# Kernel optimization log

Hardware: AMD Instinct MI355X
Metric: run time of the kernel (lower is better)

The kernel has to match this reference:

```python
import jax, jax.numpy as jnp
import numpy as np

B, L, IN_DIM, DIM, H = 1, 256, 128, 32, 4
LN_EPS = 1e-5


def setup_inputs() -> dict:
    key = jax.random.key(0)
    ks = jax.random.split(key, 7)
    z = jax.random.normal(ks[0], (B, L, L, IN_DIM), dtype=jnp.float32)
    src_mask = jax.random.randint(ks[1], (B, L), 0, 2, dtype=jnp.int32)
    ln_g = jnp.ones((IN_DIM,), jnp.float32)
    ln_b = jnp.zeros((IN_DIM,), jnp.float32)
    w_qkv = jax.random.normal(ks[2], (IN_DIM, 3 * H * DIM), jnp.float32) * 0.02
    w_pair = jax.random.normal(ks[3], (IN_DIM, H), jnp.float32) * 0.02
    w_gate = jax.random.normal(ks[4], (IN_DIM, IN_DIM), jnp.float32) * 0.02
    b_gate = jnp.zeros((IN_DIM,), jnp.float32)
    w_out = jax.random.normal(ks[5], (H * DIM, IN_DIM), jnp.float32) * 0.02
    b_out = jnp.zeros((IN_DIM,), jnp.float32)
    return dict(z=z, src_mask=src_mask, ln_g=ln_g, ln_b=ln_b, w_qkv=w_qkv,
                w_pair=w_pair, w_gate=w_gate, b_gate=b_gate, w_out=w_out, b_out=b_out)


def reference(z, src_mask, ln_g, ln_b, w_qkv, w_pair, w_gate, b_gate, w_out, b_out):
    # mask: 0 -> -1, then outer product -> (B, L, L) with entries in {-1, +1}
    m = jnp.where(src_mask == 0, -1, src_mask).astype(jnp.float32)
    attn_mask = m[:, :, None] * m[:, None, :]                      # (B, L, L)

    # LayerNorm over feature dim (biased variance, as torch)
    mu = jnp.mean(z, axis=-1, keepdims=True)
    var = jnp.mean((z - mu) ** 2, axis=-1, keepdims=True)
    zn = (z - mu) / jnp.sqrt(var + LN_EPS) * ln_g + ln_b           # (B, I, J, C)

    gate = jax.nn.sigmoid(zn @ w_gate + b_gate)                    # (B, I, J, C)
    bias = zn @ w_pair                                             # (B, I, J, H)

    qkv = zn @ w_qkv                                               # (B, I, J, 3*H*D)
    q, k, v = jnp.split(qkv, 3, axis=-1)
    q = q.reshape(B, L, L, H, DIM)
    k = k.reshape(B, L, L, H, DIM)
    v = v.reshape(B, L, L, H, DIM)

    # NOTE: original code DIVIDES by scale = d**-0.5 (i.e. multiplies by sqrt(d)).
    scale = DIM ** (-0.5)
    logits = jnp.einsum('brihd,brjhd->brijh', q, k) / scale        # (B, R, I, J, H)
    logits = logits + bias[:, None, :, :, :]
    # NOTE: original masked_fill uses -1e-9 (tiny), kept faithfully.
    logits = jnp.where(attn_mask[:, None, :, :, None] == -1, jnp.float32(-1e-9), logits)
    attn = jax.nn.softmax(logits, axis=3)                          # softmax over key j

    out = jnp.einsum('brijh,brjhd->brihd', attn, v)                # (B, R, I, H, D)
    out = out.reshape(B, L, L, H * DIM)
    return (gate * out) @ w_out + b_out                            # (B, I, J, C)
```

## Files before the change

kernel.cpp:

```cpp
#include <hip/hip_runtime.h>
#include <hip/hip_bf16.h>

#define L_DIM 256
#define C_DIM 128
#define H_DIM 4
#define D_DIM 32
#define NPOS (L_DIM * L_DIM)
#define SQRT_D 5.6568542494923806f

typedef float f32x4 __attribute__((ext_vector_type(4)));
typedef short bf16x8 __attribute__((ext_vector_type(8)));
typedef unsigned short ushort8_t __attribute__((ext_vector_type(8)));

__device__ __forceinline__ float bf2f(unsigned short u) {
  return __uint_as_float(((unsigned)u) << 16);
}
__device__ __forceinline__ unsigned short f2bf(float f) {
  unsigned u = __float_as_uint(f);
  unsigned r = u + 0x7fffu + ((u >> 16) & 1u);
  return (unsigned short)(r >> 16);
}

__global__ __launch_bounds__(256)
void k_prep(const float* __restrict__ w_qkv, const float* __restrict__ w_gate,
            const float* __restrict__ w_out,
            unsigned short* __restrict__ WcT, unsigned short* __restrict__ WoT) {
  int idx = blockIdx.x * 256 + threadIdx.x;
  if (idx < 512 * 128) {
    int n = idx >> 7, c = idx & 127;
    float v = (n < 384) ? w_qkv[c * 384 + n] : w_gate[c * 128 + (n - 384)];
    WcT[idx] = f2bf(v);
  } else if (idx < 512 * 128 + 128 * 128) {
    int i2 = idx - 512 * 128;
    int n = i2 >> 7, c = i2 & 127;
    WoT[i2] = f2bf(w_out[c * 128 + n]);
  }
}

__global__ __launch_bounds__(256)
void k_bias(const float* __restrict__ z, const float* __restrict__ ln_g,
            const float* __restrict__ ln_b, const float* __restrict__ w_pair,
            float* __restrict__ biasT) {
  int t = threadIdx.x;
  int p = blockIdx.x * 32 + (t >> 3);
  int lane = t & 7;
  const float* zp = &z[(size_t)p * C_DIM + lane * 16];
  float x[16];
  #pragma unroll
  for (int e = 0; e < 4; e++) {
    float4 v = reinterpret_cast<const float4*>(zp)[e];
    x[e * 4 + 0] = v.x; x[e * 4 + 1] = v.y; x[e * 4 + 2] = v.z; x[e * 4 + 3] = v.w;
  }
  float s = 0.f;
  #pragma unroll
  for (int e = 0; e < 16; e++) s += x[e];
  s += __shfl_xor(s, 1); s += __shfl_xor(s, 2); s += __shfl_xor(s, 4);
  float mu = s * (1.0f / C_DIM);
  float v2 = 0.f;
  #pragma unroll
  for (int e = 0; e < 16; e++) { float d = x[e] - mu; v2 += d * d; }
  v2 += __shfl_xor(v2, 1); v2 += __shfl_xor(v2, 2); v2 += __shfl_xor(v2, 4);
  float rs = rsqrtf(v2 * (1.0f / C_DIM) + 1e-5f);
  float bh[H_DIM] = {};
  #pragma unroll
  for (int e = 0; e < 16; e++) {
    int c = lane * 16 + e;
    float zn = (x[e] - mu) * rs * ln_g[c] + ln_b[c];
    #pragma unroll
    for (int h = 0; h < H_DIM; h++) bh[h] += zn * w_pair[c * H_DIM + h];
  }
  #pragma unroll
  for (int h = 0; h < H_DIM; h++) {
    bh[h] += __shfl_xor(bh[h], 1); bh[h] += __shfl_xor(bh[h], 2); bh[h] += __shfl_xor(bh[h], 4);
  }
  if (lane == 0) {
    int iz = p >> 8, jz = p & 255;
    #pragma unroll
    for (int h = 0; h < H_DIM; h++) biasT[h * NPOS + jz * L_DIM + iz] = bh[h];
  }
}

__global__ __launch_bounds__(512, 2)
void k_fused(const float* __restrict__ z, const int* __restrict__ src_mask,
             const float* __restrict__ ln_g, const float* __restrict__ ln_b,
             const float* __restrict__ b_gate, const unsigned short* __restrict__ WcT,
             const float* __restrict__ biasT, float* __restrict__ og) {
  __shared__ __align__(16) char smem[156672];
  char* zn_c = smem;
  unsigned short* Qs = (unsigned short*)(smem + 65536);
  unsigned short* Ks = (unsigned short*)(smem + 86016);
  char* Vt_c = smem + 106496;
  char* Wt_c = smem + 122880;
  int* smk   = (int*)(smem + 155648);

  const int t = threadIdx.x;
  const int wave = t >> 6, lane = t & 63;
  const int rbase = blockIdx.x * L_DIM;
  const int wrow0 = wave * 32;
  char* P_c = smem + 122880 + wave * 4096;

  {
    int ln8 = t & 7;
    for (int pass = 0; pass < 4; ++pass) {
      int pos = pass * 64 + (t >> 3);
      const float* zp = z + ((size_t)(rbase + pos)) * C_DIM + ln8 * 16;
      float x[16];
      #pragma unroll
      for (int e = 0; e < 4; e++) {
        float4 v = reinterpret_cast<const float4*>(zp)[e];
        x[e * 4 + 0] = v.x; x[e * 4 + 1] = v.y; x[e * 4 + 2] = v.z; x[e * 4 + 3] = v.w;
      }
      float s = 0.f;
      #pragma unroll
      for (int e = 0; e < 16; e++) s += x[e];
      s += __shfl_xor(s, 1); s += __shfl_xor(s, 2); s += __shfl_xor(s, 4);
      float mu = s * (1.0f / C_DIM);
      float v2 = 0.f;
      #pragma unroll
      for (int e = 0; e < 16; e++) { float d = x[e] - mu; v2 += d * d; }
      v2 += __shfl_xor(v2, 1); v2 += __shfl_xor(v2, 2); v2 += __shfl_xor(v2, 4);
      float rstd = rsqrtf(v2 * (1.0f / C_DIM) + 1e-5f);
      unsigned short hb[16];
      #pragma unroll
      for (int e = 0; e < 16; e++) {
        int c = ln8 * 16 + e;
        hb[e] = f2bf((x[e] - mu) * rstd * ln_g[c] + ln_b[c]);
      }
      uint4 w0, w1;
      w0.x = hb[0] | ((unsigned)hb[1] << 16);  w0.y = hb[2] | ((unsigned)hb[3] << 16);
      w0.z = hb[4] | ((unsigned)hb[5] << 16);  w0.w = hb[6] | ((unsigned)hb[7] << 16);
      w1.x = hb[8] | ((unsigned)hb[9] << 16);  w1.y = hb[10] | ((unsigned)hb[11] << 16);
      w1.z = hb[12] | ((unsigned)hb[13] << 16); w1.w = hb[14] | ((unsigned)hb[15] << 16);
      int sw = (pos & 7) << 4;
      *(uint4*)(zn_c + pos * 256 + ((ln8 * 32) ^ sw)) = w0;
      *(uint4*)(zn_c + pos * 256 + ((ln8 * 32 + 16) ^ sw)) = w1;
    }
    if (t < 256) smk[t] = src_mask[t];
  }

  unsigned mib = 0;

  f32x4 gacc[2][2];

  for (int h = 0; h < H_DIM; ++h) {
    {
      int row = t >> 2, q4 = t & 3;
      int src = ((row >> 5) * 128) + h * 32 + (row & 31);
      const char* gsrc = (const char*)(WcT + src * 128);
      int sw = (row & 7) << 4;
      #pragma unroll
      for (int e = 0; e < 4; e++) {
        int cb = q4 * 64 + e * 16;
        ushort8_t v = *(const ushort8_t*)(gsrc + cb);
        *(ushort8_t*)(Wt_c + row * 256 + (cb ^ sw)) = v;
      }
    }
    __syncthreads();
    if (h == 0) {
      #pragma unroll
      for (int mi = 0; mi < 2; mi++)
        #pragma unroll
        for (int q = 0; q < 4; q++) {
          int i = wrow0 + mi * 16 + (lane >> 4) * 4 + q;
          if (smk[i] == 0) mib |= 1u << (mi * 4 + q);
        }
    }

    bf16x8 afr[2][4];
    #pragma unroll
    for (int mi = 0; mi < 2; mi++)
      #pragma unroll
      for (int kk = 0; kk < 4; kk++) {
        int row = wrow0 + mi * 16 + (lane & 15);
        int cb = kk * 64 + (lane >> 4) * 16;
        afr[mi][kk] = *(const bf16x8*)(zn_c + row * 256 + (cb ^ ((row & 7) << 4)));
      }
    #pragma unroll
    for (int o = 0; o < 4; o++) {
      #pragma unroll
      for (int mi = 0; mi < 2; mi++) {
        #pragma unroll
        for (int nt = 0; nt < 2; nt++) {
          f32x4 acc = {0.f, 0.f, 0.f, 0.f};
          #pragma unroll
          for (int kk = 0; kk < 4; kk++) {
            int wr = o * 32 + nt * 16 + (lane & 15);
            int cb = kk * 64 + (lane >> 4) * 16;
            bf16x8 bfr = *(const bf16x8*)(Wt_c + wr * 256 + (cb ^ ((wr & 7) << 4)));
            acc = __builtin_amdgcn_mfma_f32_16x16x32_bf16(afr[mi][kk], bfr, acc, 0, 0, 0);
          }
          int colb = nt * 16 + (lane & 15);
          int rowb = wrow0 + mi * 16 + (lane >> 4) * 4;
          if (o == 0) {
            #pragma unroll
            for (int q = 0; q < 4; q++) Qs[(rowb + q) * 40 + colb] = f2bf(acc[q]);
          } else if (o == 1) {
            #pragma unroll
            for (int q = 0; q < 4; q++) Ks[(rowb + q) * 40 + colb] = f2bf(acc[q]);
          } else if (o == 2) {
            uint2 pv;
            pv.x = f2bf(acc[0]) | ((unsigned)f2bf(acc[1]) << 16);
            pv.y = f2bf(acc[2]) | ((unsigned)f2bf(acc[3]) << 16);
            *(uint2*)(Vt_c + colb * 512 + ((rowb * 2) ^ ((colb & 7) << 4))) = pv;
          } else {
            gacc[mi][nt] = acc;
          }
        }
      }
    }
    __syncthreads();

    float m_run[2][4], s_run[2][4];
    f32x4 o_acc[2][2];
    #pragma unroll
    for (int mi = 0; mi < 2; mi++)
      #pragma unroll
      for (int q = 0; q < 4; q++) { m_run[mi][q] = -3.0e38f; s_run[mi][q] = 0.f; }
    #pragma unroll
    for (int mi = 0; mi < 2; mi++)
      #pragma unroll
      for (int nd = 0; nd < 2; nd++) o_acc[mi][nd] = (f32x4){0.f, 0.f, 0.f, 0.f};

    bf16x8 qfr[2];
    #pragma unroll
    for (int mi = 0; mi < 2; mi++) {
      int qr = wrow0 + mi * 16 + (lane & 15);
      qfr[mi] = *(const bf16x8*)((const char*)Qs + qr * 80 + (lane >> 4) * 16);
    }
    const float* biasTh = biasT + h * NPOS;

    for (int jb = 0; jb < 4; ++jb) {
      bf16x8 kfr[4];
      #pragma unroll
      for (int ji = 0; ji < 4; ji++) {
        int jr = jb * 64 + ji * 16 + (lane & 15);
        kfr[ji] = *(const bf16x8*)((const char*)Ks + jr * 80 + (lane >> 4) * 16);
      }
      f32x4 sacc[2][4];
      #pragma unroll
      for (int mi = 0; mi < 2; mi++)
        #pragma unroll
        for (int ji = 0; ji < 4; ji++) {
          f32x4 zz = {0.f, 0.f, 0.f, 0.f};
          sacc[mi][ji] = __builtin_amdgcn_mfma_f32_16x16x32_bf16(qfr[mi], kfr[ji], zz, 0, 0, 0);
        }
      #pragma unroll
      for (int mi = 0; mi < 2; mi++) {
        #pragma unroll
        for (int ji = 0; ji < 4; ji++) {
          int j = jb * 64 + ji * 16 + (lane & 15);
          int ib = wrow0 + mi * 16 + (lane >> 4) * 4;
          float4 b4 = *(const float4*)(biasTh + j * L_DIM + ib);
          bool mjz = (smk[j] == 0);
          float bb[4] = {b4.x, b4.y, b4.z, b4.w};
          #pragma unroll
          for (int q = 0; q < 4; q++) {
            float sv = sacc[mi][ji][q] * SQRT_D + bb[q];
            bool miz = (mib >> (mi * 4 + q)) & 1u;
            if (miz != mjz) sv = -1e-9f;
            sacc[mi][ji][q] = sv;
          }
        }
      }
      #pragma unroll
      for (int mi = 0; mi < 2; mi++) {
        #pragma unroll
        for (int q = 0; q < 4; q++) {
          float v = fmaxf(fmaxf(sacc[mi][0][q], sacc[mi][1][q]),
                          fmaxf(sacc[mi][2][q], sacc[mi][3][q]));
          v = fmaxf(v, __shfl_xor(v, 1)); v = fmaxf(v, __shfl_xor(v, 2));
          v = fmaxf(v, __shfl_xor(v, 4)); v = fmaxf(v, __shfl_xor(v, 8));
          float mo = m_run[mi][q];
          float mn = fmaxf(mo, v);
          float corr = __expf(mo - mn);
          m_run[mi][q] = mn;
          float rs = 0.f;
          #pragma unroll
          for (int ji = 0; ji < 4; ji++) {
            float pp = __expf(sacc[mi][ji][q] - mn);
            sacc[mi][ji][q] = pp; rs += pp;
          }
          rs += __shfl_xor(rs, 1); rs += __shfl_xor(rs, 2);
          rs += __shfl_xor(rs, 4); rs += __shfl_xor(rs, 8);
          s_run[mi][q] = s_run[mi][q] * corr + rs;
          o_acc[mi][0][q] *= corr; o_acc[mi][1][q] *= corr;
        }
      }
      #pragma unroll
      for (int mi = 0; mi < 2; mi++)
        #pragma unroll
        for (int ji = 0; ji < 4; ji++) {
          #pragma unroll
          for (int q = 0; q < 4; q++) {
            int il = mi * 16 + (lane >> 4) * 4 + q;
            int jl = ji * 16 + (lane & 15);
            *(unsigned short*)(P_c + il * 128 + ((jl * 2) ^ ((il & 7) << 4))) =
                f2bf(sacc[mi][ji][q]);
          }
        }
      #pragma unroll
      for (int kk = 0; kk < 2; kk++) {
        bf16x8 pfr[2], vfr[2];
        #pragma unroll
        for (int mi = 0; mi < 2; mi++) {
          int pr = mi * 16 + (lane & 15);
          pfr[mi] = *(const bf16x8*)(P_c + pr * 128 +
                                     ((kk * 64 + (lane >> 4) * 16) ^ ((pr & 7) << 4)));
        }
        #pragma unroll
        for (int nd = 0; nd < 2; nd++) {
          int vr = nd * 16 + (lane & 15);
          vfr[nd] = *(const bf16x8*)(Vt_c + vr * 512 +
                                     ((jb * 128 + kk * 64 + (lane >> 4) * 16) ^ ((vr & 7) << 4)));
        }
        #pragma unroll
        for (int mi = 0; mi < 2; mi++)
          #pragma unroll
          for (int nd = 0; nd < 2; nd++)
            o_acc[mi][nd] = __builtin_amdgcn_mfma_f32_16x16x32_bf16(pfr[mi], vfr[nd],
                                                                    o_acc[mi][nd], 0, 0, 0);
      }
    }

    #pragma unroll
    for (int mi = 0; mi < 2; mi++) {
      float rcp[4];
      #pragma unroll
      for (int q = 0; q < 4; q++) rcp[q] = 1.0f / s_run[mi][q];
      #pragma unroll
      for (int nd = 0; nd < 2; nd++) {
        int c = h * 32 + nd * 16 + (lane & 15);
        float bg = b_gate[c];
        #pragma unroll
        for (int q = 0; q < 4; q++) {
          float g = 1.0f / (1.0f + __expf(-(gacc[mi][nd][q] + bg)));
          float ov = o_acc[mi][nd][q] * rcp[q] * g;
          int p = rbase + wrow0 + mi * 16 + (lane >> 4) * 4 + q;
          og[(size_t)p * C_DIM + c] = ov;
        }
      }
    }
    __syncthreads();
  }
}

__global__ __launch_bounds__(256)
void k_out(const unsigned short* __restrict__ WoT, const float* __restrict__ b_out,
           float* __restrict__ out) {
  __shared__ __align__(16) char smem[49152];
  char* Ab_c  = smem;
  char* WoT_c = smem + 16384;
  int t = threadIdx.x;
  int gr0 = blockIdx.x * 64;
  #pragma unroll
  for (int e = 0; e < 8; e++) {
    int f = t + e * 256;
    int row = f >> 5, c4 = f & 31;
    float4 v = *(const float4*)(out + (size_t)(gr0 + row) * C_DIM + c4 * 4);
    uint2 pv;
    pv.x = f2bf(v.x) | ((unsigned)f2bf(v.y) << 16);
    pv.y = f2bf(v.z) | ((unsigned)f2bf(v.w) << 16);
    *(uint2*)(Ab_c + row * 256 + ((c4 * 8) ^ ((row & 7) << 4))) = pv;
  }
  {
    int row = t >> 1, seg = t & 1;
    const char* gsrc = (const char*)(WoT + row * 128);
    int sw = (row & 7) << 4;
    #pragma unroll
    for (int e = 0; e < 8; e++) {
      int cb = seg * 128 + e * 16;
      ushort8_t v = *(const ushort8_t*)(gsrc + cb);
      *(ushort8_t*)(WoT_c + row * 256 + (cb ^ sw)) = v;
    }
  }
  __syncthreads();

  int wave = t >> 6, lane = t & 63;
  int base = wave * 16;
  bf16x8 afr[4];
  #pragma unroll
  for (int kk = 0; kk < 4; kk++) {
    int row = base + (lane & 15);
    int cb = kk * 64 + (lane >> 4) * 16;
    afr[kk] = *(const bf16x8*)(Ab_c + row * 256 + (cb ^ ((row & 7) << 4)));
  }
  f32x4 acc[8];
  #pragma unroll
  for (int nt = 0; nt < 8; nt++) {
    acc[nt] = (f32x4){0.f, 0.f, 0.f, 0.f};
    #pragma unroll
    for (int kk = 0; kk < 4; kk++) {
      int wr = nt * 16 + (lane & 15);
      int cb = kk * 64 + (lane >> 4) * 16;
      bf16x8 bfr = *(const bf16x8*)(WoT_c + wr * 256 + (cb ^ ((wr & 7) << 4)));
      acc[nt] = __builtin_amdgcn_mfma_f32_16x16x32_bf16(afr[kk], bfr, acc[nt], 0, 0, 0);
    }
  }
  __syncthreads();
  #pragma unroll
  for (int nt = 0; nt < 8; nt++) {
    int n = nt * 16 + (lane & 15);
    float bo = b_out[n];
    #pragma unroll
    for (int q = 0; q < 4; q++) {
      int p = gr0 + base + (lane >> 4) * 4 + q;
      out[(size_t)p * C_DIM + n] = acc[nt][q] + bo;
    }
  }
}

extern "C" void kernel_launch(void* const* d_in, const int* in_sizes, int n_in,
                              void* d_out, int out_size, void* d_ws, size_t ws_size,
                              hipStream_t stream) {
  const float* z      = (const float*)d_in[0];
  const int*   smask  = (const int*)  d_in[1];
  const float* ln_g   = (const float*)d_in[2];
  const float* ln_b   = (const float*)d_in[3];
  const float* w_qkv  = (const float*)d_in[4];
  const float* w_pair = (const float*)d_in[5];
  const float* w_gate = (const float*)d_in[6];
  const float* b_gate = (const float*)d_in[7];
  const float* w_out  = (const float*)d_in[8];
  const float* b_out  = (const float*)d_in[9];
  float* out = (float*)d_out;

  char* ws = (char*)d_ws;
  unsigned short* WcT   = (unsigned short*)(ws);
  unsigned short* WoT   = (unsigned short*)(ws + 131072);
  float*          biasT = (float*)(ws + 163840);
  (void)ws_size; (void)in_sizes; (void)n_in; (void)out_size;

  k_prep<<<dim3(320), dim3(256), 0, stream>>>(w_qkv, w_gate, w_out, WcT, WoT);
  k_bias<<<dim3(NPOS / 32), dim3(256), 0, stream>>>(z, ln_g, ln_b, w_pair, biasT);
  k_fused<<<dim3(L_DIM), dim3(512), 0, stream>>>(z, smask, ln_g, ln_b, b_gate, WcT, biasT, out);
  k_out<<<dim3(NPOS / 64), dim3(256), 0, stream>>>(WoT, b_out, out);
}
```

Before: 228.4 us.

## Use 1024-thread blocks, drop online-softmax max, double-buffer pre-swizzled weights

Doubles the waves per block so each wave handles 16 query rows instead of 32, improving latency hiding at one block per CU. It also removes the running-max online softmax in favour of a direct exp-and-sum with a single final normalisation. Weights are pre-swizzled per head in the prep kernel, and the next head's weights are prefetched into registers and double-buffered in LDS. The zn fragments and the mask bits are hoisted out of the head loop. Skipping max subtraction risks exp overflow if the logits grow large, and the shared-memory regions now alias, since Q, K and V reuse the zn area.

Measured after the change: 192.1 us. 1.19x faster.

```diff
diff --git a/kernel.cpp b/kernel.cpp
--- a/kernel.cpp
+++ b/kernel.cpp
@@ -4,7 +4,6 @@
 #define L_DIM 256
 #define C_DIM 128
 #define H_DIM 4
-#define D_DIM 32
 #define NPOS (L_DIM * L_DIM)
 #define SQRT_D 5.6568542494923806f
 
@@ -24,14 +23,17 @@
 __global__ __launch_bounds__(256)
 void k_prep(const float* __restrict__ w_qkv, const float* __restrict__ w_gate,
             const float* __restrict__ w_out,
-            unsigned short* __restrict__ WcT, unsigned short* __restrict__ WoT) {
+            unsigned short* __restrict__ WcS, unsigned short* __restrict__ WoT) {
   int idx = blockIdx.x * 256 + threadIdx.x;
-  if (idx < 512 * 128) {
-    int n = idx >> 7, c = idx & 127;
-    float v = (n < 384) ? w_qkv[c * 384 + n] : w_gate[c * 128 + (n - 384)];
-    WcT[idx] = f2bf(v);
-  } else if (idx < 512 * 128 + 128 * 128) {
-    int i2 = idx - 512 * 128;
+  if (idx < 4 * 128 * 128) {
+    int h = idx >> 14, rem = idx & 16383, rr = rem >> 7, c = rem & 127;
+    int o = rr >> 5, n32 = rr & 31;
+    float v = (o < 3) ? w_qkv[c * 384 + o * 128 + h * 32 + n32]
+                      : w_gate[c * 128 + h * 32 + n32];
+    int byte_in_row = (2 * c) ^ ((rr & 7) << 4);
+    WcS[h * 16384 + rr * 128 + (byte_in_row >> 1)] = f2bf(v);
+  } else if (idx < 4 * 128 * 128 + 128 * 128) {
+    int i2 = idx - 65536;
     int n = i2 >> 7, c = i2 & 127;
     WoT[i2] = f2bf(w_out[c * 128 + n]);
   }
@@ -80,29 +82,32 @@
   }
 }
 
-__global__ __launch_bounds__(512, 2)
+__global__ __launch_bounds__(1024)
 void k_fused(const float* __restrict__ z, const int* __restrict__ src_mask,
              const float* __restrict__ ln_g, const float* __restrict__ ln_b,
-             const float* __restrict__ b_gate, const unsigned short* __restrict__ WcT,
+             const float* __restrict__ b_gate, const unsigned short* __restrict__ WcS,
              const float* __restrict__ biasT, float* __restrict__ og) {
   __shared__ __align__(16) char smem[156672];
   char* zn_c = smem;
-  unsigned short* Qs = (unsigned short*)(smem + 65536);
-  unsigned short* Ks = (unsigned short*)(smem + 86016);
-  char* Vt_c = smem + 106496;
-  char* Wt_c = smem + 122880;
-  int* smk   = (int*)(smem + 155648);
+  unsigned short* Qs = (unsigned short*)(smem);
+  unsigned short* Ks = (unsigned short*)(smem + 20480);
+  char* Vt_c = smem + 40960;
+  char* P_c0 = smem + 57344;
+  char* Wt_c = smem + 90112;
+  int*  smk  = (int*)(smem + 155648);
 
   const int t = threadIdx.x;
   const int wave = t >> 6, lane = t & 63;
+  const int l15 = lane & 15, l4 = lane >> 4;
   const int rbase = blockIdx.x * L_DIM;
-  const int wrow0 = wave * 32;
-  char* P_c = smem + 122880 + wave * 4096;
+  const int wrow0 = wave * 16;
+  char* P_c = P_c0 + wave * 2048;
 
   {
     int ln8 = t & 7;
-    for (int pass = 0; pass < 4; ++pass) {
-      int pos = pass * 64 + (t >> 3);
+    #pragma unroll
+    for (int pass = 0; pass < 2; ++pass) {
+      int pos = pass * 128 + (t >> 3);
       const float* zp = z + ((size_t)(rbase + pos)) * C_DIM + ln8 * 16;
       float x[16];
       #pragma unroll
@@ -136,209 +141,141 @@
       *(uint4*)(zn_c + pos * 256 + ((ln8 * 32 + 16) ^ sw)) = w1;
     }
     if (t < 256) smk[t] = src_mask[t];
-  }
-
-  unsigned mib = 0;
-
-  f32x4 gacc[2][2];
+    const ushort8_t* src = (const ushort8_t*)WcS;
+    ushort8_t* dst = (ushort8_t*)Wt_c;
+    dst[t] = src[t];
+    dst[t + 1024] = src[t + 1024];
+  }
+  __syncthreads();
+
+  bf16x8 afr[4];
+  {
+    int row = wrow0 + l15, sw = (row & 7) << 4;
+    #pragma unroll
+    for (int kk = 0; kk < 4; kk++)
+      afr[kk] = *(const bf16x8*)(zn_c + row * 256 + ((kk * 64 + l4 * 16) ^ sw));
+  }
+  unsigned mib = 0, mjb = 0;
+  #pragma unroll
+  for (int q = 0; q < 4; q++)
+    if (smk[wrow0 + l4 * 4 + q] == 0) mib |= 1u << q;
+  #pragma unroll
+  for (int jj = 0; jj < 16; jj++)
+    if (smk[(jj >> 2) * 64 + (jj & 3) * 16 + l15] == 0) mjb |= 1u << jj;
+  __syncthreads();
 
   for (int h = 0; h < H_DIM; ++h) {
-    {
-      int row = t >> 2, q4 = t & 3;
-      int src = ((row >> 5) * 128) + h * 32 + (row & 31);
-      const char* gsrc = (const char*)(WcT + src * 128);
-      int sw = (row & 7) << 4;
-      #pragma unroll
-      for (int e = 0; e < 4; e++) {
-        int cb = q4 * 64 + e * 16;
-        ushort8_t v = *(const ushort8_t*)(gsrc + cb);
-        *(ushort8_t*)(Wt_c + row * 256 + (cb ^ sw)) = v;
+    const char* WtCur = Wt_c + (h & 1) * 32768;
+    ushort8_t ld0, ld1;
+    if (h < 3) {
+      const ushort8_t* src = (const ushort8_t*)(WcS + (h + 1) * 16384);
+      ld0 = src[t]; ld1 = src[t + 1024];
+    }
+
+    f32x4 gacc[2];
+    #pragma unroll
+    for (int o = 0; o < 4; o++) {
+      #pragma unroll
+      for (int nt = 0; nt < 2; nt++) {
+        f32x4 acc = {0.f, 0.f, 0.f, 0.f};
+        #pragma unroll
+        for (int kk = 0; kk < 4; kk++) {
+          int wr = o * 32 + nt * 16 + l15;
+          bf16x8 bfr = *(const bf16x8*)(WtCur + wr * 256 + ((kk * 64 + l4 * 16) ^ ((wr & 7) << 4)));
+          acc = __builtin_amdgcn_mfma_f32_16x16x32_bf16(afr[kk], bfr, acc, 0, 0, 0);
+        }
+        int colb = nt * 16 + l15;
+        int rowb = wrow0 + l4 * 4;
+        if (o == 0) {
+          #pragma unroll
+          for (int q = 0; q < 4; q++) Qs[(rowb + q) * 40 + colb] = f2bf(acc[q]);
+        } else if (o == 1) {
+          #pragma unroll
+          for (int q = 0; q < 4; q++) Ks[(rowb + q) * 40 + colb] = f2bf(acc[q]);
+        } else if (o == 2) {
+          uint2 pv;
+          pv.x = f2bf(acc[0]) | ((unsigned)f2bf(acc[1]) << 16);
+          pv.y = f2bf(acc[2]) | ((unsigned)f2bf(acc[3]) << 16);
+          *(uint2*)(Vt_c + colb * 512 + ((rowb * 2) ^ ((colb & 7) << 4))) = pv;
+        } else {
+          gacc[nt] = acc;
+        }
       }
     }
     __syncthreads();
-    if (h == 0) {
-      #pragma unroll
-      for (int mi = 0; mi < 2; mi++)
+
+    bf16x8 qfr = *(const bf16x8*)((const char*)Qs + (wrow0 + l15) * 80 + l4 * 16);
+    const float* biasTh = biasT + h * NPOS;
+    float s_part[4] = {0.f, 0.f, 0.f, 0.f};
+    f32x4 o_acc[2];
+    o_acc[0] = (f32x4){0.f, 0.f, 0.f, 0.f};
+    o_acc[1] = (f32x4){0.f, 0.f, 0.f, 0.f};
+
+    for (int jb = 0; jb < 4; ++jb) {
+      f32x4 sacc[4];
+      #pragma unroll
+      for (int ji = 0; ji < 4; ji++) {
+        int jr = jb * 64 + ji * 16 + l15;
+        bf16x8 kfr = *(const bf16x8*)((const char*)Ks + jr * 80 + l4 * 16);
+        f32x4 zz = {0.f, 0.f, 0.f, 0.f};
+        sacc[ji] = __builtin_amdgcn_mfma_f32_16x16x32_bf16(qfr, kfr, zz, 0, 0, 0);
+      }
+      #pragma unroll
+      for (int ji = 0; ji < 4; ji++) {
+        int j = jb * 64 + ji * 16 + l15;
+        int ib = wrow0 + l4 * 4;
+        float4 b4 = *(const float4*)(biasTh + j * L_DIM + ib);
+        bool mjz = (mjb >> (jb * 4 + ji)) & 1u;
+        float bb[4] = {b4.x, b4.y, b4.z, b4.w};
         #pragma unroll
         for (int q = 0; q < 4; q++) {
-          int i = wrow0 + mi * 16 + (lane >> 4) * 4 + q;
-          if (smk[i] == 0) mib |= 1u << (mi * 4 + q);
+          float sv = sacc[ji][q] * SQRT_D + bb[q];
+          bool miz = (mib >> q) & 1u;
+          if (miz != mjz) sv = -1e-9f;
+          float p = __expf(sv);
+          s_part[q] += p;
+          int il = l4 * 4 + q, jl = ji * 16 + l15;
+          *(unsigned short*)(P_c + il * 128 + ((jl * 2) ^ ((il & 7) << 4))) = f2bf(p);
         }
-    }
-
-    bf16x8 afr[2][4];
-    #pragma unroll
-    for (int mi = 0; mi < 2; mi++)
-      #pragma unroll
-      for (int kk = 0; kk < 4; kk++) {
-        int row = wrow0 + mi * 16 + (lane & 15);
-        int cb = kk * 64 + (lane >> 4) * 16;
-        afr[mi][kk] = *(const bf16x8*)(zn_c + row * 256 + (cb ^ ((row & 7) << 4)));
-      }
-    #pragma unroll
-    for (int o = 0; o < 4; o++) {
-      #pragma unroll
-      for (int mi = 0; mi < 2; mi++) {
-        #pragma unroll
-        for (int nt = 0; nt < 2; nt++) {
-          f32x4 acc = {0.f, 0.f, 0.f, 0.f};
-          #pragma unroll
-          for (int kk = 0; kk < 4; kk++) {
-            int wr = o * 32 + nt * 16 + (lane & 15);
-            int cb = kk * 64 + (lane >> 4) * 16;
-            bf16x8 bfr = *(const bf16x8*)(Wt_c + wr * 256 + (cb ^ ((wr & 7) << 4)));
-            acc = __builtin_amdgcn_mfma_f32_16x16x32_bf16(afr[mi][kk], bfr, acc, 0, 0, 0);
-          }
-          int colb = nt * 16 + (lane & 15);
-          int rowb = wrow0 + mi * 16 + (lane >> 4) * 4;
-          if (o == 0) {
-            #pragma unroll
-            for (int q = 0; q < 4; q++) Qs[(rowb + q) * 40 + colb] = f2bf(acc[q]);
-          } else if (o == 1) {
-            #pragma unroll
-            for (int q = 0; q < 4; q++) Ks[(rowb + q) * 40 + colb] = f2bf(acc[q]);
-          } else if (o == 2) {
-            uint2 pv;
-            pv.x = f2bf(acc[0]) | ((unsigned)f2bf(acc[1]) << 16);
-            pv.y = f2bf(acc[2]) | ((unsigned)f2bf(acc[3]) << 16);
-            *(uint2*)(Vt_c + colb * 512 + ((rowb * 2) ^ ((colb & 7) << 4))) = pv;
-          } else {
-            gacc[mi][nt] = acc;
-          }
-        }
-      }
-    }
-    __syncthreads();
-
-    float m_run[2][4], s_run[2][4];
-    f32x4 o_acc[2][2];
-    #pragma unroll
-    for (int mi = 0; mi < 2; mi++)
-      #pragma unroll
-      for (int q = 0; q < 4; q++) { m_run[mi][q] = -3.0e38f; s_run[mi][q] = 0.f; }
-    #pragma unroll
-    for (int mi = 0; mi < 2; mi++)
-      #pragma unroll
-      for (int nd = 0; nd < 2; nd++) o_acc[mi][nd] = (f32x4){0.f, 0.f, 0.f, 0.f};
-
-    bf16x8 qfr[2];
-    #pragma unroll
-    for (int mi = 0; mi < 2; mi++) {
-      int qr = wrow0 + mi * 16 + (lane & 15);
-      qfr[mi] = *(const bf16x8*)((const char*)Qs + qr * 80 + (lane >> 4) * 16);
-    }
-    const float* biasTh = biasT + h * NPOS;
-
-    for (int jb = 0; jb < 4; ++jb) {
-      bf16x8 kfr[4];
-      #pragma unroll
-      for (int ji = 0; ji < 4; ji++) {
-        int jr = jb * 64 + ji * 16 + (lane & 15);
-        kfr[ji] = *(const bf16x8*)((const char*)Ks + jr * 80 + (lane >> 4) * 16);
-      }
-      f32x4 sacc[2][4];
-      #pragma unroll
-      for (int mi = 0; mi < 2; mi++)
-        #pragma unroll
-        for (int ji = 0; ji < 4; ji++) {
-          f32x4 zz = {0.f, 0.f, 0.f, 0.f};
-          sacc[mi][ji] = __builtin_amdgcn_mfma_f32_16x16x32_bf16(qfr[mi], kfr[ji], zz, 0, 0, 0);
-        }
-      #pragma unroll
-      for (int mi = 0; mi < 2; mi++) {
-        #pragma unroll
-        for (int ji = 0; ji < 4; ji++) {
-          int j = jb * 64 + ji * 16 + (lane & 15);
-          int ib = wrow0 + mi * 16 + (lane >> 4) * 4;
-          float4 b4 = *(const float4*)(biasTh + j * L_DIM + ib);
-          bool mjz = (smk[j] == 0);
-          float bb[4] = {b4.x, b4.y, b4.z, b4.w};
-          #pragma unroll
-          for (int q = 0; q < 4; q++) {
-            float sv = sacc[mi][ji][q] * SQRT_D + bb[q];
-            bool miz = (mib >> (mi * 4 + q)) & 1u;
-            if (miz != mjz) sv = -1e-9f;
-            sacc[mi][ji][q] = sv;
-          }
-        }
-      }
-      #pragma unroll
-      for (int mi = 0; mi < 2; mi++) {
-        #pragma unroll
-        for (int q = 0; q < 4; q++) {
-          float v = fmaxf(fmaxf(sacc[mi][0][q], sacc[mi][1][q]),
-                          fmaxf(sacc[mi][2][q], sacc[mi][3][q]));
-          v = fmaxf(v, __shfl_xor(v, 1)); v = fmaxf(v, __shfl_xor(v, 2));
-          v = fmaxf(v, __shfl_xor(v, 4)); v = fmaxf(v, __shfl_xor(v, 8));
-          float mo = m_run[mi][q];
-          float mn = fmaxf(mo, v);
-          float corr = __expf(mo - mn);
-          m_run[mi][q] = mn;
-          float rs = 0.f;
-          #pragma unroll
-          for (int ji = 0; ji < 4; ji++) {
-            float pp = __expf(sacc[mi][ji][q] - mn);
-            sacc[mi][ji][q] = pp; rs += pp;
-          }
-          rs += __shfl_xor(rs, 1); rs += __shfl_xor(rs, 2);
-          rs += __shfl_xor(rs, 4); rs += __shfl_xor(rs, 8);
-          s_run[mi][q] = s_run[mi][q] * corr + rs;
-          o_acc[mi][0][q] *= corr; o_acc[mi][1][q] *= corr;
-        }
-      }
-      #pragma unroll
-      for (int mi = 0; mi < 2; mi++)
-        #pragma unroll
-        for (int ji = 0; ji < 4; ji++) {
-          #pragma unroll
-          for (int q = 0; q < 4; q++) {
-            int il = mi * 16 + (lane >> 4) * 4 + q;
-            int jl = ji * 16 + (lane & 15);
-            *(unsigned short*)(P_c + il * 128 + ((jl * 2) ^ ((il & 7) << 4))) =
-                f2bf(sacc[mi][ji][q]);
-          }
-        }
+      }
       #pragma unroll
       for (int kk = 0; kk < 2; kk++) {
-        bf16x8 pfr[2], vfr[2];
-        #pragma unroll
-        for (int mi = 0; mi < 2; mi++) {
-          int pr = mi * 16 + (lane & 15);
-          pfr[mi] = *(const bf16x8*)(P_c + pr * 128 +
-                                     ((kk * 64 + (lane >> 4) * 16) ^ ((pr & 7) << 4)));
-        }
+        bf16x8 pfr = *(const bf16x8*)(P_c + l15 * 128 + ((kk * 64 + l4 * 16) ^ ((l15 & 7) << 4)));
         #pragma unroll
         for (int nd = 0; nd < 2; nd++) {
-          int vr = nd * 16 + (lane & 15);
-          vfr[nd] = *(const bf16x8*)(Vt_c + vr * 512 +
-                                     ((jb * 128 + kk * 64 + (lane >> 4) * 16) ^ ((vr & 7) << 4)));
+          int vr = nd * 16 + l15;
+          bf16x8 vfr = *(const bf16x8*)(Vt_c + vr * 512 +
+                                        ((jb * 128 + kk * 64 + l4 * 16) ^ ((vr & 7) << 4)));
+          o_acc[nd] = __builtin_amdgcn_mfma_f32_16x16x32_bf16(pfr, vfr, o_acc[nd], 0, 0, 0);
         }
-        #pragma unroll
-        for (int mi = 0; mi < 2; mi++)
-          #pragma unroll
-          for (int nd = 0; nd < 2; nd++)
-            o_acc[mi][nd] = __builtin_amdgcn_mfma_f32_16x16x32_bf16(pfr[mi], vfr[nd],
-                                                                    o_acc[mi][nd], 0, 0, 0);
-      }
-    }
-
-    #pragma unroll
-    for (int mi = 0; mi < 2; mi++) {
-      float rcp[4];
-      #pragma unroll
-      for (int q = 0; q < 4; q++) rcp[q] = 1.0f / s_run[mi][q];
-      #pragma unroll
-      for (int nd = 0; nd < 2; nd++) {
-        int c = h * 32 + nd * 16 + (lane & 15);
-        float bg = b_gate[c];
-        #pragma unroll
-        for (int q = 0; q < 4; q++) {
-          float g = 1.0f / (1.0f + __expf(-(gacc[mi][nd][q] + bg)));
-          float ov = o_acc[mi][nd][q] * rcp[q] * g;
-          int p = rbase + wrow0 + mi * 16 + (lane >> 4) * 4 + q;
-          og[(size_t)p * C_DIM + c] = ov;
-        }
-      }
+      }
+    }
+
+    #pragma unroll
+    for (int q = 0; q < 4; q++) {
+      float s = s_part[q];
+      s += __shfl_xor(s, 1); s += __shfl_xor(s, 2);
+      s += __shfl_xor(s, 4); s += __shfl_xor(s, 8);
+      s_part[q] = s;
+    }
+
+    #pragma unroll
+    for (int nd = 0; nd < 2; nd++) {
+      int c = h * 32 + nd * 16 + l15;
+      float bg = b_gate[c];
+      #pragma unroll
+      for (int q = 0; q < 4; q++) {
+        float g = 1.0f / (1.0f + __expf(-(gacc[nd][q] + bg)));
+        float ov = o_acc[nd][q] * (1.0f / s_part[q]) * g;
+        int p = rbase + wrow0 + l4 * 4 + q;
+        og[(size_t)p * C_DIM + c] = ov;
+      }
+    }
+
+    if (h < 3) {
+      ushort8_t* dst = (ushort8_t*)(Wt_c + ((h + 1) & 1) * 32768);
+      dst[t] = ld0;
+      dst[t + 1024] = ld1;
     }
     __syncthreads();
   }
@@ -425,13 +362,13 @@
   float* out = (float*)d_out;
 
   char* ws = (char*)d_ws;
-  unsigned short* WcT   = (unsigned short*)(ws);
+  unsigned short* WcS   = (unsigned short*)(ws);
   unsigned short* WoT   = (unsigned short*)(ws + 131072);
   float*          biasT = (float*)(ws + 163840);
   (void)ws_size; (void)in_sizes; (void)n_in; (void)out_size;
 
-  k_prep<<<dim3(320), dim3(256), 0, stream>>>(w_qkv, w_gate, w_out, WcT, WoT);
+  k_prep<<<dim3(320), dim3(256), 0, stream>>>(w_qkv, w_gate, w_out, WcS, WoT);
   k_bias<<<dim3(NPOS / 32), dim3(256), 0, stream>>>(z, ln_g, ln_b, w_pair, biasT);
-  k_fused<<<dim3(L_DIM), dim3(512), 0, stream>>>(z, smask, ln_g, ln_b, b_gate, WcT, biasT, out);
+  k_fused<<<dim3(L_DIM), dim3(1024), 0, stream>>>(z, smask, ln_g, ln_b, b_gate, WcS, biasT, out);
   k_out<<<dim3(NPOS / 64), dim3(256), 0, stream>>>(WoT, b_out, out);
 }
```
